# Performance work log

Hardware: AMD Instinct MI355X
Metric: run time of the kernel (lower is better)

## Reference

```python
import jax, jax.numpy as jnp
import numpy as np

K = 64          # settings['k']
GAMMA = 2.0     # 1 / (2 * length_scale^2), length_scale = 0.5


def setup_inputs() -> dict:
    key = jax.random.key(0)
    ks = jax.random.split(key, 8)
    B, L, F, H = 1024, 512, 256, 512
    inputs = jax.random.normal(ks[0], (B, L, F), dtype=jnp.float32)
    coords = jax.random.uniform(ks[1], (B, L, 2), dtype=jnp.float32)
    targets = jax.random.normal(ks[2], (B, L, 1), dtype=jnp.float32)
    input_lengths = jnp.full((B,), L, dtype=jnp.int32)
    # GraphSAGE (PyG) params: SAGEConv has lin_l (on aggregated, with bias)
    # and lin_r (on root, no bias). kaiming-normal-ish init per original.
    s1 = float(np.sqrt(2.0 / F))
    s2 = float(np.sqrt(2.0 / H))
    W1l = jax.random.normal(ks[3], (H, F), dtype=jnp.float32) * s1
    W1r = jax.random.normal(ks[4], (H, F), dtype=jnp.float32) * s1
    b1 = jnp.zeros((H,), dtype=jnp.float32)
    W2l = jax.random.normal(ks[5], (1, H), dtype=jnp.float32) * s2
    W2r = jax.random.normal(ks[6], (1, H), dtype=jnp.float32) * s2
    b2 = jnp.zeros((1,), dtype=jnp.float32)
    return {"inputs": inputs, "coords": coords, "targets": targets,
            "input_lengths": input_lengths,
            "W1l": W1l, "W1r": W1r, "b1": b1,
            "W2l": W2l, "W2r": W2r, "b2": b2}


def _gather_nodes(inp, coo, tar, inp_l):
    # Per-sample KNN: query = point 0, candidates = points 1..L-1.
    q = coo[0]                                    # [2]
    d2 = jnp.sum((coo[1:] - q) ** 2, axis=-1)     # [L-1]
    pos = jnp.arange(d2.shape[0])
    d2 = jnp.where(pos < inp_l - 1, d2, jnp.inf)  # mask padding
    _, nbr = jax.lax.top_k(-d2, K)                # K nearest, sorted by dist
    # Faithful to the original code: the sklearn neighbor indices (relative to
    # coo[1:]) are used to index the FULL arrays inp/tar/coo (no +1 offset).
    x = jnp.concatenate([inp[:1], inp[nbr]], axis=0)  # [K+1, F]
    y = jnp.concatenate([tar[:1], tar[nbr]], axis=0)  # [K+1, 1]
    return x, y


def reference(inputs, coords, targets, input_lengths, W1l, W1r, b1, W2l, W2r, b2):
    # Build per-sample node sets. [B, K+1, F], [B, K+1, 1]
    x, y = jax.vmap(_gather_nodes)(inputs, coords, targets, input_lengths)
    # RBF adjacency exp(-GAMMA*||ci-cj||^2) is strictly positive, so nonzero()
    # yields the COMPLETE graph with self-loops on each (K+1)-node sample.
    # PyG SAGEConv ignores edge_weight, so mean aggregation = mean over all
    # K+1 nodes of the sample (identical for every node in the sample).
    aggr1 = jnp.mean(x, axis=1, keepdims=True)                 # [B,1,F]
    h = jax.nn.relu(aggr1 @ W1l.T + x @ W1r.T + b1)            # [B,K+1,H]
    aggr2 = jnp.mean(h, axis=1, keepdims=True)                 # [B,1,H]
    out = aggr2 @ W2l.T + h @ W2r.T + b2                       # [B,K+1,1]
    # head_only=True: first node (the query) per batch element
    return out[:, 0, :], y[:, 0, :]
```

## Files before the change

kernel.cpp:

```cpp
#include <hip/hip_runtime.h>
#include <hip/hip_bf16.h>
#include <stdint.h>

typedef __attribute__((ext_vector_type(8))) __bf16 bf16x8;
typedef __attribute__((ext_vector_type(4))) float f32x4;
typedef __attribute__((ext_vector_type(2))) float f32x2;

#define NBATCH 1024
#define SEQL   512
#define FDIM   256
#define HDIM   512
#define KNN    64
#define NODES  65
#define ROWSTR 512

__device__ __forceinline__ unsigned short f32_bf16(float f) {
    unsigned int u = __float_as_uint(f);
    unsigned int r = u + 0x7FFFu + ((u >> 16) & 1u);
    return (unsigned short)(r >> 16);
}

__global__ __launch_bounds__(256) void convw_kernel(
    const float* __restrict__ W1r, const float* __restrict__ W1l,
    unsigned short* __restrict__ Wb)
{
    int i = blockIdx.x * 256 + threadIdx.x;
    int f = i * 8;
    int row = f >> 8;
    int col = f & 255;
    int mat = row >> 9;
    int r   = row & 511;
    int j   = col >> 3;
    int g   = j & 3, kidx = j >> 2;
    int cl  = r & 15, cb16 = r >> 4;
    int lane = g * 16 + cl;

    const float* src = (mat ? W1l : W1r) + (size_t)r * FDIM + col;
    float4 a = *reinterpret_cast<const float4*>(src);
    float4 c = *reinterpret_cast<const float4*>(src + 4);
    uint4 t;
    t.x = (unsigned)f32_bf16(a.x) | ((unsigned)f32_bf16(a.y) << 16);
    t.y = (unsigned)f32_bf16(a.z) | ((unsigned)f32_bf16(a.w) << 16);
    t.z = (unsigned)f32_bf16(c.x) | ((unsigned)f32_bf16(c.y) << 16);
    t.w = (unsigned)f32_bf16(c.z) | ((unsigned)f32_bf16(c.w) << 16);

    size_t tchunk = (size_t)((mat * 32 + cb16) * 8 + kidx) * 64 + lane;
    *reinterpret_cast<uint4*>(Wb + tchunk * 8) = t;
}

__global__ __launch_bounds__(512, 4) void fused_kernel(
    const float* __restrict__ inputs,
    const float* __restrict__ coords,
    const float* __restrict__ targets,
    const int*   __restrict__ lens,
    const unsigned short* __restrict__ Wb,
    const float* __restrict__ b1,
    const float* __restrict__ W2l,
    const float* __restrict__ W2r,
    const float* __restrict__ b2,
    float* __restrict__ dout)
{
    __shared__ unsigned long long keys[512];
    __shared__ int idxs[KNN];
    __shared__ __align__(16) float4 part[8][64];
    __shared__ __align__(16) unsigned short ldsA[66 * FDIM];

    const int b   = blockIdx.x;
    const int tid = threadIdx.x;
    const float* cb = coords + (size_t)b * (SEQL * 2);
    const float qx = cb[0], qy = cb[1];
    const int len = lens[b];

    unsigned long long key;
    if (tid < SEQL - 1 && tid < len - 1) {
        f32x2 c2 = __builtin_nontemporal_load(
            reinterpret_cast<const f32x2*>(cb + 2 * (tid + 1)));
        float dx = c2[0] - qx;
        float dy = c2[1] - qy;
        float d2 = dx * dx + dy * dy;
        key = ((unsigned long long)__float_as_uint(d2) << 32) | (unsigned int)tid;
    } else {
        key = ~0ull;
    }

    for (int k = 2; k <= 512; k <<= 1) {
        for (int j = k >> 1; j >= 64; j >>= 1) {
            keys[tid] = key;
            __syncthreads();
            unsigned long long other = keys[tid ^ j];
            bool takemin = (((tid & j) == 0) == ((tid & k) == 0));
            key = (takemin == (key < other)) ? key : other;
            __syncthreads();
        }
        for (int j = ((k >> 1) > 32 ? 32 : (k >> 1)); j >= 1; j >>= 1) {
            unsigned long long other = __shfl_xor(key, j, 64);
            bool takemin = (((tid & j) == 0) == ((tid & k) == 0));
            key = (takemin == (key < other)) ? key : other;
        }
    }

    if (tid < KNN) idxs[tid] = (int)(unsigned int)(key & 0xffffffffull);
    if (tid == 0) {
        dout[b] = b2[0];
        dout[NBATCH + b] = targets[(size_t)b * SEQL];
    }
    __syncthreads();

    const int c4 = tid & 63;
    const int g0 = tid >> 6;

#define STROW(row, v) do {                                                     \
    int off_ = (row) * ROWSTR + c4 * 8; off_ ^= ((row) & 7) << 4;              \
    uint2 pk_;                                                                 \
    pk_.x = (unsigned)f32_bf16((v)[0]) | ((unsigned)f32_bf16((v)[1]) << 16);   \
    pk_.y = (unsigned)f32_bf16((v)[2]) | ((unsigned)f32_bf16((v)[3]) << 16);   \
    *reinterpret_cast<uint2*>(reinterpret_cast<char*>(ldsA) + off_) = pk_;     \
} while (0)

    {
        const float* xb = inputs + (size_t)b * SEQL * FDIM + c4 * 4;
        int srcs[8];
        #pragma unroll
        for (int q = 0; q < 8; ++q) {
            int r = g0 + q * 8;
            srcs[q] = (r == 0) ? 0 : idxs[r - 1];
        }
        int src8 = idxs[63];
        f32x4 v[8];
        #pragma unroll
        for (int q = 0; q < 8; ++q)
            v[q] = __builtin_nontemporal_load(
                reinterpret_cast<const f32x4*>(xb + (size_t)srcs[q] * FDIM));
        f32x4 v8;
        if (g0 == 0)
            v8 = __builtin_nontemporal_load(
                reinterpret_cast<const f32x4*>(xb + (size_t)src8 * FDIM));

        float4 sum = {0.f, 0.f, 0.f, 0.f};
        #pragma unroll
        for (int q = 0; q < 8; ++q) {
            int r = g0 + q * 8;
            sum.x += v[q][0]; sum.y += v[q][1]; sum.z += v[q][2]; sum.w += v[q][3];
            STROW(r, v[q]);
        }
        if (g0 == 0) {
            sum.x += v8[0]; sum.y += v8[1]; sum.z += v8[2]; sum.w += v8[3];
            STROW(64, v8);
        }
        part[g0][c4] = sum;
    }
    __syncthreads();
    if (tid < 64) {
        float sx = 0.f, sy = 0.f, sz = 0.f, sw = 0.f;
        #pragma unroll
        for (int q = 0; q < 8; ++q) {
            float4 p = part[q][tid];
            sx += p.x; sy += p.y; sz += p.z; sw += p.w;
        }
        const float inv = 1.0f / 65.0f;
        uint2 pk;
        pk.x = (unsigned)f32_bf16(sx * inv) | ((unsigned)f32_bf16(sy * inv) << 16);
        pk.y = (unsigned)f32_bf16(sz * inv) | ((unsigned)f32_bf16(sw * inv) << 16);
        int off = 65 * ROWSTR + tid * 8; off ^= 0x10;
        *reinterpret_cast<uint2*>(reinterpret_cast<char*>(ldsA) + off) = pk;
    }
    __syncthreads();
#undef STROW

    const int lane = tid & 63;
    const int w    = tid >> 6;
    const int cl   = lane & 15, g = lane >> 4;

    #pragma unroll
    for (int p = 0; p < 2; ++p) {
        const int cbase = w * 64 + p * 32;

        f32x4 acc[5][2], accU[2];
        #pragma unroll
        for (int m = 0; m < 5; ++m) {
            acc[m][0] = f32x4{0.f, 0.f, 0.f, 0.f};
            acc[m][1] = f32x4{0.f, 0.f, 0.f, 0.f};
        }
        accU[0] = f32x4{0.f, 0.f, 0.f, 0.f};
        accU[1] = f32x4{0.f, 0.f, 0.f, 0.f};

        const int blkR = w * 4 + p * 2;
        const char* base = (const char*)Wb;
        const size_t oR0 = (size_t)(blkR * 8) * 1024 + (size_t)lane * 16;
        const size_t oR1 = oR0 + 8 * 1024;
        const size_t oL0 = oR0 + (size_t)32 * 8 * 1024;
        const size_t oL1 = oL0 + 8 * 1024;

        #pragma unroll
        for (int kc = 0; kc < 4; ++kc) {
            #pragma unroll
            for (int s = 0; s < 2; ++s) {
                const int kb  = kc * 128 + s * 64;
                const int kfr = (kc * 2 + s) * 1024;
                bf16x8 bR[2], bL[2], aF[5];
                bR[0] = *reinterpret_cast<const bf16x8*>(base + oR0 + kfr);
                bR[1] = *reinterpret_cast<const bf16x8*>(base + oR1 + kfr);
                bL[0] = *reinterpret_cast<const bf16x8*>(base + oL0 + kfr);
                bL[1] = *reinterpret_cast<const bf16x8*>(base + oL1 + kfr);
                #pragma unroll
                for (int m = 0; m < 5; ++m) {
                    int row = m * 16 + cl;
                    int off = row * ROWSTR + kb + g * 16;
                    off ^= (row & 7) << 4;
                    aF[m] = *reinterpret_cast<const bf16x8*>(
                        reinterpret_cast<const char*>(ldsA) + off);
                }
                #pragma unroll
                for (int m = 0; m < 5; ++m) {
                    acc[m][0] = __builtin_amdgcn_mfma_f32_16x16x32_bf16(
                        aF[m], bR[0], acc[m][0], 0, 0, 0);
                    acc[m][1] = __builtin_amdgcn_mfma_f32_16x16x32_bf16(
                        aF[m], bR[1], acc[m][1], 0, 0, 0);
                }
                accU[0] = __builtin_amdgcn_mfma_f32_16x16x32_bf16(
                    aF[4], bL[0], accU[0], 0, 0, 0);
                accU[1] = __builtin_amdgcn_mfma_f32_16x16x32_bf16(
                    aF[4], bL[1], accU[1], 0, 0, 0);
            }
        }

        float contrib = 0.f;
        #pragma unroll
        for (int nf = 0; nf < 2; ++nf) {
            int c = cbase + nf * 16 + cl;
            float wl  = W2l[c] * (1.0f / 65.0f);
            float w2  = W2r[c];
            float uc  = __shfl(accU[nf][1], cl, 64) + b1[c];
            float ps = 0.f;
            #pragma unroll
            for (int m = 0; m < 4; ++m)
                #pragma unroll
                for (int v = 0; v < 4; ++v)
                    ps += fmaxf(acc[m][nf][v] + uc, 0.f);
            {
                float hh = fmaxf(acc[4][nf][0] + uc, 0.f);
                ps += (g == 0) ? hh : 0.f;
            }
            contrib += wl * ps;
            if (g == 0) {
                float h0 = fmaxf(acc[0][nf][0] + uc, 0.f);
                contrib += w2 * h0;
            }
        }
        #pragma unroll
        for (int mask = 1; mask < 64; mask <<= 1)
            contrib += __shfl_xor(contrib, mask, 64);
        if (lane == 0) atomicAdd(&dout[b], contrib);
    }
}

extern "C" void kernel_launch(void* const* d_in, const int* in_sizes, int n_in,
                              void* d_out, int out_size, void* d_ws, size_t ws_size,
                              hipStream_t stream) {
    const float* inputs  = (const float*)d_in[0];
    const float* coords  = (const float*)d_in[1];
    const float* targets = (const float*)d_in[2];
    const int*   lens    = (const int*)d_in[3];
    const float* W1l     = (const float*)d_in[4];
    const float* W1r     = (const float*)d_in[5];
    const float* b1      = (const float*)d_in[6];
    const float* W2l     = (const float*)d_in[7];
    const float* W2r     = (const float*)d_in[8];
    const float* b2      = (const float*)d_in[9];
    float* dout = (float*)d_out;

    unsigned short* Wb = (unsigned short*)d_ws;

    convw_kernel<<<dim3(2 * HDIM * FDIM / (256 * 8)), dim3(256), 0, stream>>>(
        W1r, W1l, Wb);

    fused_kernel<<<dim3(NBATCH), dim3(512), 0, stream>>>(
        inputs, coords, targets, lens, Wb, b1, W2l, W2r, b2, dout);
}
```

Baseline: 62.91 us.

## Halve fused kernel block to 256 threads with two keys per thread

Each block of the fused kernel now runs 256 threads instead of 512. In the bitonic sort every thread holds two keys, and the j=256 stage becomes an in-register compare. The gather loop and the GEMM loop now cover twice the rows and columns per thread or wave, and the sort keys and partial sums share one LDS union buffer to cut shared memory. The aim is more resident blocks per CU and fewer block-wide barriers, at the cost of less parallelism inside each block and longer serial loops per wave.

```diff
diff --git a/kernel.cpp b/kernel.cpp
--- a/kernel.cpp
+++ b/kernel.cpp
@@ -48,7 +48,7 @@
     *reinterpret_cast<uint4*>(Wb + tchunk * 8) = t;
 }
 
-__global__ __launch_bounds__(512, 4) void fused_kernel(
+__global__ __launch_bounds__(256, 4) void fused_kernel(
     const float* __restrict__ inputs,
     const float* __restrict__ coords,
     const float* __restrict__ targets,
@@ -60,46 +60,66 @@
     const float* __restrict__ b2,
     float* __restrict__ dout)
 {
-    __shared__ unsigned long long keys[512];
+    __shared__ __align__(16) unsigned short ldsA[66 * FDIM];
+    __shared__ __align__(16) unsigned char uni[4096];
     __shared__ int idxs[KNN];
-    __shared__ __align__(16) float4 part[8][64];
-    __shared__ __align__(16) unsigned short ldsA[66 * FDIM];
-
-    const int b   = blockIdx.x;
-    const int tid = threadIdx.x;
+
+    const int b    = blockIdx.x;
+    const int tid  = threadIdx.x;
+    const int lane = tid & 63;
+
     const float* cb = coords + (size_t)b * (SEQL * 2);
     const float qx = cb[0], qy = cb[1];
     const int len = lens[b];
 
-    unsigned long long key;
+    unsigned long long* keys = reinterpret_cast<unsigned long long*>(uni);
+    unsigned long long k0 = ~0ull, k1 = ~0ull;
     if (tid < SEQL - 1 && tid < len - 1) {
         f32x2 c2 = __builtin_nontemporal_load(
             reinterpret_cast<const f32x2*>(cb + 2 * (tid + 1)));
-        float dx = c2[0] - qx;
-        float dy = c2[1] - qy;
+        float dx = c2[0] - qx, dy = c2[1] - qy;
         float d2 = dx * dx + dy * dy;
-        key = ((unsigned long long)__float_as_uint(d2) << 32) | (unsigned int)tid;
-    } else {
-        key = ~0ull;
+        k0 = ((unsigned long long)__float_as_uint(d2) << 32) | (unsigned int)tid;
+    }
+    {
+        int c1 = tid + 256;
+        if (c1 < SEQL - 1 && c1 < len - 1) {
+            f32x2 c2 = __builtin_nontemporal_load(
+                reinterpret_cast<const f32x2*>(cb + 2 * (c1 + 1)));
+            float dx = c2[0] - qx, dy = c2[1] - qy;
+            float d2 = dx * dx + dy * dy;
+            k1 = ((unsigned long long)__float_as_uint(d2) << 32) | (unsigned int)c1;
+        }
     }
 
     for (int k = 2; k <= 512; k <<= 1) {
-        for (int j = k >> 1; j >= 64; j >>= 1) {
-            keys[tid] = key;
-            __syncthreads();
-            unsigned long long other = keys[tid ^ j];
-            bool takemin = (((tid & j) == 0) == ((tid & k) == 0));
-            key = (takemin == (key < other)) ? key : other;
-            __syncthreads();
-        }
-        for (int j = ((k >> 1) > 32 ? 32 : (k >> 1)); j >= 1; j >>= 1) {
-            unsigned long long other = __shfl_xor(key, j, 64);
-            bool takemin = (((tid & j) == 0) == ((tid & k) == 0));
-            key = (takemin == (key < other)) ? key : other;
-        }
-    }
-
-    if (tid < KNN) idxs[tid] = (int)(unsigned int)(key & 0xffffffffull);
+        for (int j = k >> 1; j >= 1; j >>= 1) {
+            if (j == 256) {
+                unsigned long long lo = (k0 < k1) ? k0 : k1;
+                unsigned long long hi = (k0 < k1) ? k1 : k0;
+                k0 = lo; k1 = hi;
+            } else if (j >= 64) {
+                keys[tid] = k0; keys[tid + 256] = k1;
+                __syncthreads();
+                unsigned long long o0 = keys[tid ^ j];
+                unsigned long long o1 = keys[(tid ^ j) + 256];
+                bool t0 = (((tid & j) == 0) == ((tid & k) == 0));
+                bool t1 = (((tid & j) == 0) == (((tid + 256) & k) == 0));
+                k0 = (t0 == (k0 < o0)) ? k0 : o0;
+                k1 = (t1 == (k1 < o1)) ? k1 : o1;
+                __syncthreads();
+            } else {
+                unsigned long long o0 = __shfl_xor(k0, j, 64);
+                unsigned long long o1 = __shfl_xor(k1, j, 64);
+                bool t0 = (((tid & j) == 0) == ((tid & k) == 0));
+                bool t1 = (((tid & j) == 0) == (((tid + 256) & k) == 0));
+                k0 = (t0 == (k0 < o0)) ? k0 : o0;
+                k1 = (t1 == (k1 < o1)) ? k1 : o1;
+            }
+        }
+    }
+
+    if (tid < KNN) idxs[tid] = (int)(unsigned int)(k0 & 0xffffffffull);
     if (tid == 0) {
         dout[b] = b2[0];
         dout[NBATCH + b] = targets[(size_t)b * SEQL];
@@ -119,42 +139,45 @@
 
     {
         const float* xb = inputs + (size_t)b * SEQL * FDIM + c4 * 4;
-        int srcs[8];
-        #pragma unroll
-        for (int q = 0; q < 8; ++q) {
-            int r = g0 + q * 8;
-            srcs[q] = (r == 0) ? 0 : idxs[r - 1];
-        }
-        int src8 = idxs[63];
-        f32x4 v[8];
-        #pragma unroll
-        for (int q = 0; q < 8; ++q)
-            v[q] = __builtin_nontemporal_load(
-                reinterpret_cast<const f32x4*>(xb + (size_t)srcs[q] * FDIM));
-        f32x4 v8;
-        if (g0 == 0)
-            v8 = __builtin_nontemporal_load(
-                reinterpret_cast<const f32x4*>(xb + (size_t)src8 * FDIM));
-
         float4 sum = {0.f, 0.f, 0.f, 0.f};
-        #pragma unroll
-        for (int q = 0; q < 8; ++q) {
-            int r = g0 + q * 8;
-            sum.x += v[q][0]; sum.y += v[q][1]; sum.z += v[q][2]; sum.w += v[q][3];
-            STROW(r, v[q]);
+        #pragma unroll 1
+        for (int half = 0; half < 2; ++half) {
+            int srcs[8];
+            #pragma unroll
+            for (int q = 0; q < 8; ++q) {
+                int r = g0 + (half * 8 + q) * 4;
+                srcs[q] = (r == 0) ? 0 : idxs[r - 1];
+            }
+            f32x4 v[8];
+            #pragma unroll
+            for (int q = 0; q < 8; ++q)
+                v[q] = __builtin_nontemporal_load(
+                    reinterpret_cast<const f32x4*>(xb + (size_t)srcs[q] * FDIM));
+            #pragma unroll
+            for (int q = 0; q < 8; ++q) {
+                int r = g0 + (half * 8 + q) * 4;
+                sum.x += v[q][0]; sum.y += v[q][1];
+                sum.z += v[q][2]; sum.w += v[q][3];
+                STROW(r, v[q]);
+            }
         }
         if (g0 == 0) {
+            f32x4 v8 = __builtin_nontemporal_load(
+                reinterpret_cast<const f32x4*>(xb + (size_t)idxs[63] * FDIM));
             sum.x += v8[0]; sum.y += v8[1]; sum.z += v8[2]; sum.w += v8[3];
             STROW(64, v8);
         }
-        part[g0][c4] = sum;
+        __syncthreads();
+        float4* part = reinterpret_cast<float4*>(uni);
+        part[g0 * 64 + c4] = sum;
     }
     __syncthreads();
     if (tid < 64) {
+        const float4* part = reinterpret_cast<const float4*>(uni);
         float sx = 0.f, sy = 0.f, sz = 0.f, sw = 0.f;
         #pragma unroll
-        for (int q = 0; q < 8; ++q) {
-            float4 p = part[q][tid];
+        for (int q = 0; q < 4; ++q) {
+            float4 p = part[q * 64 + tid];
             sx += p.x; sy += p.y; sz += p.z; sw += p.w;
         }
         const float inv = 1.0f / 65.0f;
@@ -167,13 +190,12 @@
     __syncthreads();
 #undef STROW
 
-    const int lane = tid & 63;
-    const int w    = tid >> 6;
-    const int cl   = lane & 15, g = lane >> 4;
-
-    #pragma unroll
-    for (int p = 0; p < 2; ++p) {
-        const int cbase = w * 64 + p * 32;
+    const int w  = tid >> 6;
+    const int cl = lane & 15, g = lane >> 4;
+
+    #pragma unroll 1
+    for (int p = 0; p < 4; ++p) {
+        const int cbase = w * 128 + p * 32;
 
         f32x4 acc[5][2], accU[2];
         #pragma unroll
@@ -184,7 +206,7 @@
         accU[0] = f32x4{0.f, 0.f, 0.f, 0.f};
         accU[1] = f32x4{0.f, 0.f, 0.f, 0.f};
 
-        const int blkR = w * 4 + p * 2;
+        const int blkR = w * 8 + p * 2;
         const char* base = (const char*)Wb;
         const size_t oR0 = (size_t)(blkR * 8) * 1024 + (size_t)lane * 16;
         const size_t oR1 = oR0 + 8 * 1024;
@@ -274,6 +296,6 @@
     convw_kernel<<<dim3(2 * HDIM * FDIM / (256 * 8)), dim3(256), 0, stream>>>(
         W1r, W1l, Wb);
 
-    fused_kernel<<<dim3(NBATCH), dim3(512), 0, stream>>>(
+    fused_kernel<<<dim3(NBATCH), dim3(256), 0, stream>>>(
         inputs, coords, targets, lens, Wb, b1, W2l, W2r, b2, dout);
 }
```

New measurement: 148.5 us. 136% more time.

## Split fused kernel into KNN-gather and GEMM kernels via workspace tiles

Applied to the files above, without the earlier changes.

Splits the single fused kernel into two launches. The first does the KNN sort and gather, writing bf16 node tiles into workspace, with higher occupancy (launch bounds 512,8) and reduced shared memory, since the partial-sum buffer now reuses the keys array. The second loads those tiles into LDS and runs the MFMA GEMM and reduction. This separates the latency-bound sort/gather phase from the compute phase so each gets suitable occupancy, at the cost of an extra round trip of roughly 34 MB through global memory and one more launch. The old fused kernel is kept as a fallback when the workspace is too small.

```diff
diff --git a/kernel.cpp b/kernel.cpp
--- a/kernel.cpp
+++ b/kernel.cpp
@@ -5,6 +5,7 @@
 typedef __attribute__((ext_vector_type(8))) __bf16 bf16x8;
 typedef __attribute__((ext_vector_type(4))) float f32x4;
 typedef __attribute__((ext_vector_type(2))) float f32x2;
+typedef __attribute__((ext_vector_type(4))) unsigned int u32x4;
 
 #define NBATCH 1024
 #define SEQL   512
@@ -13,6 +14,8 @@
 #define KNN    64
 #define NODES  65
 #define ROWSTR 512
+#define TILE_SHORTS 16896
+#define TILE_U4     2112
 
 __device__ __forceinline__ unsigned short f32_bf16(float f) {
     unsigned int u = __float_as_uint(f);
@@ -48,21 +51,14 @@
     *reinterpret_cast<uint4*>(Wb + tchunk * 8) = t;
 }
 
-__global__ __launch_bounds__(512, 4) void fused_kernel(
+__global__ __launch_bounds__(512, 8) void knn_gather_kernel(
     const float* __restrict__ inputs,
     const float* __restrict__ coords,
-    const float* __restrict__ targets,
     const int*   __restrict__ lens,
-    const unsigned short* __restrict__ Wb,
-    const float* __restrict__ b1,
-    const float* __restrict__ W2l,
-    const float* __restrict__ W2r,
-    const float* __restrict__ b2,
-    float* __restrict__ dout)
+    unsigned short* __restrict__ tiles)
 {
-    __shared__ unsigned long long keys[512];
+    __shared__ __align__(16) unsigned long long keys[512];
     __shared__ int idxs[KNN];
-    __shared__ __align__(16) float4 part[8][64];
     __shared__ __align__(16) unsigned short ldsA[66 * FDIM];
 
     const int b   = blockIdx.x;
@@ -100,10 +96,6 @@
     }
 
     if (tid < KNN) idxs[tid] = (int)(unsigned int)(key & 0xffffffffull);
-    if (tid == 0) {
-        dout[b] = b2[0];
-        dout[NBATCH + b] = targets[(size_t)b * SEQL];
-    }
     __syncthreads();
 
     const int c4 = tid & 63;
@@ -117,44 +109,57 @@
     *reinterpret_cast<uint2*>(reinterpret_cast<char*>(ldsA) + off_) = pk_;     \
 } while (0)
 
+    float4 sum = {0.f, 0.f, 0.f, 0.f};
     {
         const float* xb = inputs + (size_t)b * SEQL * FDIM + c4 * 4;
-        int srcs[8];
-        #pragma unroll
-        for (int q = 0; q < 8; ++q) {
-            int r = g0 + q * 8;
-            srcs[q] = (r == 0) ? 0 : idxs[r - 1];
-        }
-        int src8 = idxs[63];
-        f32x4 v[8];
-        #pragma unroll
-        for (int q = 0; q < 8; ++q)
-            v[q] = __builtin_nontemporal_load(
-                reinterpret_cast<const f32x4*>(xb + (size_t)srcs[q] * FDIM));
-        f32x4 v8;
-        if (g0 == 0)
-            v8 = __builtin_nontemporal_load(
-                reinterpret_cast<const f32x4*>(xb + (size_t)src8 * FDIM));
-
-        float4 sum = {0.f, 0.f, 0.f, 0.f};
-        #pragma unroll
-        for (int q = 0; q < 8; ++q) {
-            int r = g0 + q * 8;
-            sum.x += v[q][0]; sum.y += v[q][1]; sum.z += v[q][2]; sum.w += v[q][3];
-            STROW(r, v[q]);
+        #pragma unroll 1
+        for (int kk = 0; kk < 8; kk += 4) {
+            int srcs[4];
+            #pragma unroll
+            for (int q = 0; q < 4; ++q) {
+                int r = g0 + (kk + q) * 8;
+                srcs[q] = (r == 0) ? 0 : idxs[r - 1];
+            }
+            f32x4 v[4];
+            #pragma unroll
+            for (int q = 0; q < 4; ++q)
+                v[q] = __builtin_nontemporal_load(
+                    reinterpret_cast<const f32x4*>(xb + (size_t)srcs[q] * FDIM));
+            #pragma unroll
+            for (int q = 0; q < 4; ++q) {
+                int r = g0 + (kk + q) * 8;
+                sum.x += v[q][0]; sum.y += v[q][1];
+                sum.z += v[q][2]; sum.w += v[q][3];
+                STROW(r, v[q]);
+            }
         }
         if (g0 == 0) {
+            f32x4 v8 = __builtin_nontemporal_load(
+                reinterpret_cast<const f32x4*>(xb + (size_t)idxs[63] * FDIM));
             sum.x += v8[0]; sum.y += v8[1]; sum.z += v8[2]; sum.w += v8[3];
             STROW(64, v8);
         }
-        part[g0][c4] = sum;
-    }
-    __syncthreads();
+    }
+
+    float4* part4 = reinterpret_cast<float4*>(keys);
+    __syncthreads();
+    if (g0 < 4) part4[g0 * 64 + c4] = *reinterpret_cast<float4*>(&sum);
+    __syncthreads();
+    float sx = 0.f, sy = 0.f, sz = 0.f, sw = 0.f;
     if (tid < 64) {
-        float sx = 0.f, sy = 0.f, sz = 0.f, sw = 0.f;
-        #pragma unroll
-        for (int q = 0; q < 8; ++q) {
-            float4 p = part[q][tid];
+        #pragma unroll
+        for (int q = 0; q < 4; ++q) {
+            float4 p = part4[q * 64 + tid];
+            sx += p.x; sy += p.y; sz += p.z; sw += p.w;
+        }
+    }
+    __syncthreads();
+    if (g0 >= 4) part4[(g0 - 4) * 64 + c4] = *reinterpret_cast<float4*>(&sum);
+    __syncthreads();
+    if (tid < 64) {
+        #pragma unroll
+        for (int q = 0; q < 4; ++q) {
+            float4 p = part4[q * 64 + tid];
             sx += p.x; sy += p.y; sz += p.z; sw += p.w;
         }
         const float inv = 1.0f / 65.0f;
@@ -166,6 +171,40 @@
     }
     __syncthreads();
 #undef STROW
+
+    const u32x4* src = reinterpret_cast<const u32x4*>(ldsA);
+    u32x4* dst = reinterpret_cast<u32x4*>(tiles + (size_t)b * TILE_SHORTS);
+    for (int i = tid; i < TILE_U4; i += 512)
+        __builtin_nontemporal_store(src[i], dst + i);
+}
+
+__global__ __launch_bounds__(512, 4) void gemm_kernel(
+    const unsigned short* __restrict__ tiles,
+    const unsigned short* __restrict__ Wb,
+    const float* __restrict__ b1,
+    const float* __restrict__ W2l,
+    const float* __restrict__ W2r,
+    const float* __restrict__ b2,
+    const float* __restrict__ targets,
+    float* __restrict__ dout)
+{
+    __shared__ __align__(16) unsigned short ldsA[80 * FDIM];
+
+    const int b   = blockIdx.x;
+    const int tid = threadIdx.x;
+
+    if (tid == 0) {
+        dout[b] = b2[0];
+        dout[NBATCH + b] = targets[(size_t)b * SEQL];
+    }
+    {
+        const u32x4* src = reinterpret_cast<const u32x4*>(
+            tiles + (size_t)b * TILE_SHORTS);
+        u32x4* dst = reinterpret_cast<u32x4*>(ldsA);
+        for (int i = tid; i < TILE_U4; i += 512)
+            dst[i] = __builtin_nontemporal_load(src + i);
+    }
+    __syncthreads();
 
     const int lane = tid & 63;
     const int w    = tid >> 6;
@@ -254,6 +293,207 @@
     }
 }
 
+__global__ __launch_bounds__(512, 4) void fused_kernel(
+    const float* __restrict__ inputs, const float* __restrict__ coords,
+    const float* __restrict__ targets, const int* __restrict__ lens,
+    const unsigned short* __restrict__ Wb, const float* __restrict__ b1,
+    const float* __restrict__ W2l, const float* __restrict__ W2r,
+    const float* __restrict__ b2, float* __restrict__ dout)
+{
+    __shared__ unsigned long long keys[512];
+    __shared__ int idxs[KNN];
+    __shared__ __align__(16) float4 part[8][64];
+    __shared__ __align__(16) unsigned short ldsA[66 * FDIM];
+
+    const int b   = blockIdx.x;
+    const int tid = threadIdx.x;
+    const float* cb = coords + (size_t)b * (SEQL * 2);
+    const float qx = cb[0], qy = cb[1];
+    const int len = lens[b];
+
+    unsigned long long key;
+    if (tid < SEQL - 1 && tid < len - 1) {
+        f32x2 c2 = __builtin_nontemporal_load(
+            reinterpret_cast<const f32x2*>(cb + 2 * (tid + 1)));
+        float dx = c2[0] - qx;
+        float dy = c2[1] - qy;
+        float d2 = dx * dx + dy * dy;
+        key = ((unsigned long long)__float_as_uint(d2) << 32) | (unsigned int)tid;
+    } else {
+        key = ~0ull;
+    }
+
+    for (int k = 2; k <= 512; k <<= 1) {
+        for (int j = k >> 1; j >= 64; j >>= 1) {
+            keys[tid] = key;
+            __syncthreads();
+            unsigned long long other = keys[tid ^ j];
+            bool takemin = (((tid & j) == 0) == ((tid & k) == 0));
+            key = (takemin == (key < other)) ? key : other;
+            __syncthreads();
+        }
+        for (int j = ((k >> 1) > 32 ? 32 : (k >> 1)); j >= 1; j >>= 1) {
+            unsigned long long other = __shfl_xor(key, j, 64);
+            bool takemin = (((tid & j) == 0) == ((tid & k) == 0));
+            key = (takemin == (key < other)) ? key : other;
+        }
+    }
+
+    if (tid < KNN) idxs[tid] = (int)(unsigned int)(key & 0xffffffffull);
+    if (tid == 0) {
+        dout[b] = b2[0];
+        dout[NBATCH + b] = targets[(size_t)b * SEQL];
+    }
+    __syncthreads();
+
+    const int c4 = tid & 63;
+    const int g0 = tid >> 6;
+
+#define STROW(row, v) do {                                                     \
+    int off_ = (row) * ROWSTR + c4 * 8; off_ ^= ((row) & 7) << 4;              \
+    uint2 pk_;                                                                 \
+    pk_.x = (unsigned)f32_bf16((v)[0]) | ((unsigned)f32_bf16((v)[1]) << 16);   \
+    pk_.y = (unsigned)f32_bf16((v)[2]) | ((unsigned)f32_bf16((v)[3]) << 16);   \
+    *reinterpret_cast<uint2*>(reinterpret_cast<char*>(ldsA) + off_) = pk_;     \
+} while (0)
+
+    {
+        const float* xb = inputs + (size_t)b * SEQL * FDIM + c4 * 4;
+        int srcs[8];
+        #pragma unroll
+        for (int q = 0; q < 8; ++q) {
+            int r = g0 + q * 8;
+            srcs[q] = (r == 0) ? 0 : idxs[r - 1];
+        }
+        int src8 = idxs[63];
+        f32x4 v[8];
+        #pragma unroll
+        for (int q = 0; q < 8; ++q)
+            v[q] = __builtin_nontemporal_load(
+                reinterpret_cast<const f32x4*>(xb + (size_t)srcs[q] * FDIM));
+        f32x4 v8;
+        if (g0 == 0)
+            v8 = __builtin_nontemporal_load(
+                reinterpret_cast<const f32x4*>(xb + (size_t)src8 * FDIM));
+
+        float4 sum = {0.f, 0.f, 0.f, 0.f};
+        #pragma unroll
+        for (int q = 0; q < 8; ++q) {
+            int r = g0 + q * 8;
+            sum.x += v[q][0]; sum.y += v[q][1]; sum.z += v[q][2]; sum.w += v[q][3];
+            STROW(r, v[q]);
+        }
+        if (g0 == 0) {
+            sum.x += v8[0]; sum.y += v8[1]; sum.z += v8[2]; sum.w += v8[3];
+            STROW(64, v8);
+        }
+        part[g0][c4] = sum;
+    }
+    __syncthreads();
+    if (tid < 64) {
+        float sx = 0.f, sy = 0.f, sz = 0.f, sw = 0.f;
+        #pragma unroll
+        for (int q = 0; q < 8; ++q) {
+            float4 p = part[q][tid];
+            sx += p.x; sy += p.y; sz += p.z; sw += p.w;
+        }
+        const float inv = 1.0f / 65.0f;
+        uint2 pk;
+        pk.x = (unsigned)f32_bf16(sx * inv) | ((unsigned)f32_bf16(sy * inv) << 16);
+        pk.y = (unsigned)f32_bf16(sz * inv) | ((unsigned)f32_bf16(sw * inv) << 16);
+        int off = 65 * ROWSTR + tid * 8; off ^= 0x10;
+        *reinterpret_cast<uint2*>(reinterpret_cast<char*>(ldsA) + off) = pk;
+    }
+    __syncthreads();
+#undef STROW
+
+    const int lane = tid & 63;
+    const int w    = tid >> 6;
+    const int cl   = lane & 15, g = lane >> 4;
+
+    #pragma unroll
+    for (int p = 0; p < 2; ++p) {
+        const int cbase = w * 64 + p * 32;
+
+        f32x4 acc[5][2], accU[2];
+        #pragma unroll
+        for (int m = 0; m < 5; ++m) {
+            acc[m][0] = f32x4{0.f, 0.f, 0.f, 0.f};
+            acc[m][1] = f32x4{0.f, 0.f, 0.f, 0.f};
+        }
+        accU[0] = f32x4{0.f, 0.f, 0.f, 0.f};
+        accU[1] = f32x4{0.f, 0.f, 0.f, 0.f};
+
+        const int blkR = w * 4 + p * 2;
+        const char* base = (const char*)Wb;
+        const size_t oR0 = (size_t)(blkR * 8) * 1024 + (size_t)lane * 16;
+        const size_t oR1 = oR0 + 8 * 1024;
+        const size_t oL0 = oR0 + (size_t)32 * 8 * 1024;
+        const size_t oL1 = oL0 + 8 * 1024;
+
+        #pragma unroll
+        for (int kc = 0; kc < 4; ++kc) {
+            #pragma unroll
+            for (int s = 0; s < 2; ++s) {
+                const int kb  = kc * 128 + s * 64;
+                const int kfr = (kc * 2 + s) * 1024;
+                bf16x8 bR[2], bL[2], aF[5];
+                bR[0] = *reinterpret_cast<const bf16x8*>(base + oR0 + kfr);
+                bR[1] = *reinterpret_cast<const bf16x8*>(base + oR1 + kfr);
+                bL[0] = *reinterpret_cast<const bf16x8*>(base + oL0 + kfr);
+                bL[1] = *reinterpret_cast<const bf16x8*>(base + oL1 + kfr);
+                #pragma unroll
+                for (int m = 0; m < 5; ++m) {
+                    int row = m * 16 + cl;
+                    int off = row * ROWSTR + kb + g * 16;
+                    off ^= (row & 7) << 4;
+                    aF[m] = *reinterpret_cast<const bf16x8*>(
+                        reinterpret_cast<const char*>(ldsA) + off);
+                }
+                #pragma unroll
+                for (int m = 0; m < 5; ++m) {
+                    acc[m][0] = __builtin_amdgcn_mfma_f32_16x16x32_bf16(
+                        aF[m], bR[0], acc[m][0], 0, 0, 0);
+                    acc[m][1] = __builtin_amdgcn_mfma_f32_16x16x32_bf16(
+                        aF[m], bR[1], acc[m][1], 0, 0, 0);
+                }
+                accU[0] = __builtin_amdgcn_mfma_f32_16x16x32_bf16(
+                    aF[4], bL[0], accU[0], 0, 0, 0);
+                accU[1] = __builtin_amdgcn_mfma_f32_16x16x32_bf16(
+                    aF[4], bL[1], accU[1], 0, 0, 0);
+            }
+        }
+
+        float contrib = 0.f;
+        #pragma unroll
+        for (int nf = 0; nf < 2; ++nf) {
+            int c = cbase + nf * 16 + cl;
+            float wl  = W2l[c] * (1.0f / 65.0f);
+            float w2  = W2r[c];
+            float uc  = __shfl(accU[nf][1], cl, 64) + b1[c];
+            float ps = 0.f;
+            #pragma unroll
+            for (int m = 0; m < 4; ++m)
+                #pragma unroll
+                for (int v = 0; v < 4; ++v)
+                    ps += fmaxf(acc[m][nf][v] + uc, 0.f);
+            {
+                float hh = fmaxf(acc[4][nf][0] + uc, 0.f);
+                ps += (g == 0) ? hh : 0.f;
+            }
+            contrib += wl * ps;
+            if (g == 0) {
+                float h0 = fmaxf(acc[0][nf][0] + uc, 0.f);
+                contrib += w2 * h0;
+            }
+        }
+        #pragma unroll
+        for (int mask = 1; mask < 64; mask <<= 1)
+            contrib += __shfl_xor(contrib, mask, 64);
+        if (lane == 0) atomicAdd(&dout[b], contrib);
+    }
+}
+
 extern "C" void kernel_launch(void* const* d_in, const int* in_sizes, int n_in,
                               void* d_out, int out_size, void* d_ws, size_t ws_size,
                               hipStream_t stream) {
@@ -270,10 +510,19 @@
     float* dout = (float*)d_out;
 
     unsigned short* Wb = (unsigned short*)d_ws;
+    const size_t needed = 512 * 1024 + (size_t)NBATCH * TILE_SHORTS * 2;
 
     convw_kernel<<<dim3(2 * HDIM * FDIM / (256 * 8)), dim3(256), 0, stream>>>(
         W1r, W1l, Wb);
 
-    fused_kernel<<<dim3(NBATCH), dim3(512), 0, stream>>>(
-        inputs, coords, targets, lens, Wb, b1, W2l, W2r, b2, dout);
+    if (ws_size >= needed) {
+        unsigned short* tiles = (unsigned short*)((char*)d_ws + 512 * 1024);
+        knn_gather_kernel<<<dim3(NBATCH), dim3(512), 0, stream>>>(
+            inputs, coords, lens, tiles);
+        gemm_kernel<<<dim3(NBATCH), dim3(512), 0, stream>>>(
+            tiles, Wb, b1, W2l, W2r, b2, targets, dout);
+    } else {
+        fused_kernel<<<dim3(NBATCH), dim3(512), 0, stream>>>(
+            inputs, coords, targets, lens, Wb, b1, W2l, W2r, b2, dout);
+    }
 }
```

After: 74.92 us. +19.1%, slower.
